# Kernel tuning notes

Hardware: AMD Instinct MI355X
Metric: run time of the kernel (lower is better)

The kernel has to match this reference:

```python
import jax, jax.numpy as jnp
import numpy as np

# Faithful translations of the torch lambdas:
# r0: identity; r90: transpose(-2,-1); r180: flip(-2); r270: transpose(-2,-1) then flip(-1)
_r0 = lambda xi: xi
_r90 = lambda xi: jnp.swapaxes(xi, -2, -1)
_r180 = lambda xi: jnp.flip(xi, axis=-2)
_r270 = lambda xi: jnp.flip(jnp.swapaxes(xi, -2, -1), axis=-1)


def setup_inputs() -> dict:
    key = jax.random.key(0)
    kx, kl = jax.random.split(key)
    B, C, H, W = 256, 3, 224, 224  # square spatial required by transpose-in-place semantics
    x = jax.random.normal(kx, (B, C, H, W), dtype=jnp.float32)
    label = jax.random.randint(kl, (B,), 0, 4, dtype=jnp.int32)
    return {"x": x, "label": label}


def reference(x, label):
    # Single fused per-sample-indexed rotation via vmap + lax.switch —
    # replaces the python loop / per-sample kernel launches of the original.
    def rotate_one(xi, li):
        return jax.lax.switch(li, [_r0, _r90, _r180, _r270], xi)

    out = jax.vmap(rotate_one)(x, label)
    return (out, label)
```

## Files before the change

kernel.cpp:

```cpp
#include <hip/hip_runtime.h>


#define HW   224
#define TILE 32
#define NT   7
#define ROW4 56

__global__ __launch_bounds__(256) void rot4_band(const float* __restrict__ x,
                                                 const int* __restrict__ label,
                                                 float* __restrict__ out,
                                                 int nimg_blocks, int B) {
    const int i = blockIdx.x;
    const int t = threadIdx.x;

    if (i >= nimg_blocks) {
        const size_t img_elems = (size_t)B * 3 * HW * HW;
        if (t < B) out[img_elems + t] = (float)label[t];
        return;
    }

    int tmp = i;
    const int band = tmp % NT; tmp /= NT;
    const int c    = tmp % 3;  tmp /= 3;
    const int b    = tmp;

    const int lab = label[b];
    const size_t plane = (size_t)(b * 3 + c) * (HW * HW);
    const float* __restrict__ in = x + plane;
    float* __restrict__ o = out + plane;

    const int h0 = band * TILE;

    if (lab == 0 || lab == 2) {
#pragma unroll
        for (int k = 0; k < NT; ++k) {
            const int idx = k * 256 + t;
            const int r   = idx / ROW4;
            const int c4  = idx % ROW4;
            const int orow = h0 + r;
            const int irow = (lab == 0) ? orow : (HW - 1 - orow);
            float4 v = *(const float4*)(in + (size_t)irow * HW + c4 * 4);
            *(float4*)(o + (size_t)orow * HW + c4 * 4) = v;
        }
    } else {
        __shared__ float tb[NT][TILE][TILE + 1];
        const int wl = t >> 3;
        const int c4 = t & 7;
#pragma unroll
        for (int k = 0; k < NT; ++k) {
            const int rbase = (lab == 1) ? k * TILE : (HW - TILE - k * TILE);
            float4 v = *(const float4*)(in + (size_t)(rbase + wl) * HW + h0 + c4 * 4);
            tb[k][wl][c4 * 4 + 0] = v.x;
            tb[k][wl][c4 * 4 + 1] = v.y;
            tb[k][wl][c4 * 4 + 2] = v.z;
            tb[k][wl][c4 * 4 + 3] = v.w;
        }
        __syncthreads();
#pragma unroll
        for (int k = 0; k < NT; ++k) {
            float4 w;
            if (lab == 1) {
                w.x = tb[k][c4 * 4 + 0][wl];
                w.y = tb[k][c4 * 4 + 1][wl];
                w.z = tb[k][c4 * 4 + 2][wl];
                w.w = tb[k][c4 * 4 + 3][wl];
            } else {
                w.x = tb[k][31 - (c4 * 4 + 0)][wl];
                w.y = tb[k][31 - (c4 * 4 + 1)][wl];
                w.z = tb[k][31 - (c4 * 4 + 2)][wl];
                w.w = tb[k][31 - (c4 * 4 + 3)][wl];
            }
            *(float4*)(o + (size_t)(h0 + wl) * HW + k * TILE + c4 * 4) = w;
        }
    }
}

extern "C" void kernel_launch(void* const* d_in, const int* in_sizes, int n_in,
                              void* d_out, int out_size, void* d_ws, size_t ws_size,
                              hipStream_t stream) {
    const float* x     = (const float*)d_in[0];
    const int*   label = (const int*)d_in[1];
    float*       out   = (float*)d_out;

    const int B = in_sizes[1];
    const int nimg_blocks = B * 3 * NT;
    const int nblocks = nimg_blocks + 1;

    rot4_band<<<nblocks, 256, 0, stream>>>(x, label, out, nimg_blocks, B);
}
```

Before: 264.5 us.

## Assign one 32x32 tile per wavefront and drop block-wide barrier

Work is redistributed so each 64-lane wavefront processes a single 32x32 tile, with four tiles per block, instead of a block processing a full 32-row band of seven tiles. The transpose path uses a per-wave shared-memory slice, relying on wavefront lockstep instead of __syncthreads, and the shared footprint shrinks. This aims to raise occupancy and remove barrier stalls, at the cost of fewer loads in flight per thread and more blocks.

```diff
diff --git a/kernel.cpp b/kernel.cpp
--- a/kernel.cpp
+++ b/kernel.cpp
@@ -4,73 +4,86 @@
 #define HW   224
 #define TILE 32
 #define NT   7
-#define ROW4 56
 
-__global__ __launch_bounds__(256) void rot4_band(const float* __restrict__ x,
+__global__ __launch_bounds__(256) void rot4_wave(const float* __restrict__ x,
                                                  const int* __restrict__ label,
                                                  float* __restrict__ out,
                                                  int nimg_blocks, int B) {
-    const int i = blockIdx.x;
     const int t = threadIdx.x;
 
-    if (i >= nimg_blocks) {
+    if (blockIdx.x >= nimg_blocks) {
         const size_t img_elems = (size_t)B * 3 * HW * HW;
         if (t < B) out[img_elems + t] = (float)label[t];
         return;
     }
 
-    int tmp = i;
-    const int band = tmp % NT; tmp /= NT;
-    const int c    = tmp % 3;  tmp /= 3;
-    const int b    = tmp;
+    __shared__ float tb[4][TILE][TILE + 1];
+
+    const int wave = t >> 6;
+    const int lane = t & 63;
+
+    int g = blockIdx.x * 4 + wave;
+    const int tw = g % NT; g /= NT;
+    const int th = g % NT; g /= NT;
+    const int c  = g % 3;  g /= 3;
+    const int b  = g;
 
     const int lab = label[b];
     const size_t plane = (size_t)(b * 3 + c) * (HW * HW);
     const float* __restrict__ in = x + plane;
     float* __restrict__ o = out + plane;
 
-    const int h0 = band * TILE;
+    const int h0 = th * TILE;
+    const int w0 = tw * TILE;
+
+    const int lr = lane >> 3;
+    const int c4 = lane & 7;
 
     if (lab == 0 || lab == 2) {
+        float4 v[4];
 #pragma unroll
-        for (int k = 0; k < NT; ++k) {
-            const int idx = k * 256 + t;
-            const int r   = idx / ROW4;
-            const int c4  = idx % ROW4;
-            const int orow = h0 + r;
-            const int irow = (lab == 0) ? orow : (HW - 1 - orow);
-            float4 v = *(const float4*)(in + (size_t)irow * HW + c4 * 4);
-            *(float4*)(o + (size_t)orow * HW + c4 * 4) = v;
+        for (int i = 0; i < 4; ++i) {
+            const int r = i * 8 + lr;
+            const int irow = (lab == 0) ? (h0 + r) : (HW - 1 - (h0 + r));
+            v[i] = *(const float4*)(in + (size_t)irow * HW + w0 + c4 * 4);
+        }
+#pragma unroll
+        for (int i = 0; i < 4; ++i) {
+            const int r = i * 8 + lr;
+            *(float4*)(o + (size_t)(h0 + r) * HW + w0 + c4 * 4) = v[i];
         }
     } else {
-        __shared__ float tb[NT][TILE][TILE + 1];
-        const int wl = t >> 3;
-        const int c4 = t & 7;
+        const int rbase = (lab == 1) ? w0 : (HW - TILE - w0);
+        float4 v[4];
 #pragma unroll
-        for (int k = 0; k < NT; ++k) {
-            const int rbase = (lab == 1) ? k * TILE : (HW - TILE - k * TILE);
-            float4 v = *(const float4*)(in + (size_t)(rbase + wl) * HW + h0 + c4 * 4);
-            tb[k][wl][c4 * 4 + 0] = v.x;
-            tb[k][wl][c4 * 4 + 1] = v.y;
-            tb[k][wl][c4 * 4 + 2] = v.z;
-            tb[k][wl][c4 * 4 + 3] = v.w;
+        for (int i = 0; i < 4; ++i) {
+            const int r = i * 8 + lr;
+            v[i] = *(const float4*)(in + (size_t)(rbase + r) * HW + h0 + c4 * 4);
         }
-        __syncthreads();
 #pragma unroll
-        for (int k = 0; k < NT; ++k) {
+        for (int i = 0; i < 4; ++i) {
+            const int r = i * 8 + lr;
+            tb[wave][r][c4 * 4 + 0] = v[i].x;
+            tb[wave][r][c4 * 4 + 1] = v[i].y;
+            tb[wave][r][c4 * 4 + 2] = v[i].z;
+            tb[wave][r][c4 * 4 + 3] = v[i].w;
+        }
+#pragma unroll
+        for (int i = 0; i < 4; ++i) {
+            const int r = i * 8 + lr;
             float4 w;
             if (lab == 1) {
-                w.x = tb[k][c4 * 4 + 0][wl];
-                w.y = tb[k][c4 * 4 + 1][wl];
-                w.z = tb[k][c4 * 4 + 2][wl];
-                w.w = tb[k][c4 * 4 + 3][wl];
+                w.x = tb[wave][c4 * 4 + 0][r];
+                w.y = tb[wave][c4 * 4 + 1][r];
+                w.z = tb[wave][c4 * 4 + 2][r];
+                w.w = tb[wave][c4 * 4 + 3][r];
             } else {
-                w.x = tb[k][31 - (c4 * 4 + 0)][wl];
-                w.y = tb[k][31 - (c4 * 4 + 1)][wl];
-                w.z = tb[k][31 - (c4 * 4 + 2)][wl];
-                w.w = tb[k][31 - (c4 * 4 + 3)][wl];
+                w.x = tb[wave][31 - (c4 * 4 + 0)][r];
+                w.y = tb[wave][31 - (c4 * 4 + 1)][r];
+                w.z = tb[wave][31 - (c4 * 4 + 2)][r];
+                w.w = tb[wave][31 - (c4 * 4 + 3)][r];
             }
-            *(float4*)(o + (size_t)(h0 + wl) * HW + k * TILE + c4 * 4) = w;
+            *(float4*)(o + (size_t)(h0 + r) * HW + w0 + c4 * 4) = w;
         }
     }
 }
@@ -83,8 +96,9 @@
     float*       out   = (float*)d_out;
 
     const int B = in_sizes[1];
-    const int nimg_blocks = B * 3 * NT;
+    const int ntiles = B * 3 * NT * NT;
+    const int nimg_blocks = ntiles / 4;
     const int nblocks = nimg_blocks + 1;
 
-    rot4_band<<<nblocks, 256, 0, stream>>>(x, label, out, nimg_blocks, B);
+    rot4_wave<<<nblocks, 256, 0, stream>>>(x, label, out, nimg_blocks, B);
 }
```

Result: no change. 262.3 us (-0.8%).
